# Kernel optimization log

Hardware: AMD Instinct MI355X
Metric: run time of the kernel (lower is better)

## Reference

```python
import jax, jax.numpy as jnp
import numpy as np

NUM_LAYER = 4
EMB = 64
ATOM_VOCAB = 64
BOND_VOCAB = 8
BN_EPS = 1e-5


def _batchnorm(h, gamma, beta):
    m = h.mean(axis=0)
    v = h.var(axis=0)
    return gamma * (h - m) * jax.lax.rsqrt(v + BN_EPS) + beta


def setup_inputs() -> dict:
    key = jax.random.key(0)
    ks = jax.random.split(key, 16)
    N, E, L = 100000, 1000000, NUM_LAYER
    x = jax.random.randint(ks[0], (N, 9), 0, ATOM_VOCAB)
    edge_index = jax.random.randint(ks[1], (2, E), 0, N)
    edge_attr = jax.random.randint(ks[2], (E, 3), 0, BOND_VOCAB)
    batch = jnp.sort(jax.random.randint(ks[3], (N,), 0, 512))
    s = 0.02
    atom_emb = jax.random.normal(ks[4], (9, ATOM_VOCAB, EMB), jnp.float32) * s
    bond_emb = jax.random.normal(ks[5], (L, 3, BOND_VOCAB, EMB), jnp.float32) * s
    eps = jnp.zeros((L,), jnp.float32)
    W1 = jax.random.normal(ks[6], (L, EMB, 2 * EMB), jnp.float32) * s
    b1 = jnp.zeros((L, 2 * EMB), jnp.float32)
    bn1_g = jnp.ones((L, 2 * EMB), jnp.float32)
    bn1_b = jnp.zeros((L, 2 * EMB), jnp.float32)
    W2 = jax.random.normal(ks[7], (L, 2 * EMB, EMB), jnp.float32) * s
    b2 = jnp.zeros((L, EMB), jnp.float32)
    bn_g = jnp.ones((L, EMB), jnp.float32)
    bn_b = jnp.zeros((L, EMB), jnp.float32)
    return dict(x=x, edge_index=edge_index, edge_attr=edge_attr, batch=batch,
                atom_emb=atom_emb, bond_emb=bond_emb, eps=eps,
                W1=W1, b1=b1, bn1_g=bn1_g, bn1_b=bn1_b,
                W2=W2, b2=b2, bn_g=bn_g, bn_b=bn_b)


def reference(x, edge_index, edge_attr, batch, atom_emb, bond_emb, eps,
              W1, b1, bn1_g, bn1_b, W2, b2, bn_g, bn_b):
    N = x.shape[0]
    src, dst = edge_index[0], edge_index[1]
    # AtomEncoder: sum embeddings over the 9 atom-feature columns
    h = sum(atom_emb[c][x[:, c]] for c in range(9))  # [N, EMB]
    for layer in range(NUM_LAYER):
        # BondEncoder for this layer
        ee = sum(bond_emb[layer, c][edge_attr[:, c]] for c in range(3))  # [E, EMB]
        # message: relu(x_j + edge_emb); aggregate: scatter-add at dst
        msg = jax.nn.relu(h[src] + ee)
        agg = jax.ops.segment_sum(msg, dst, num_segments=N)
        z = (1.0 + eps[layer]) * h + agg
        # MLP: Linear -> BN -> ReLU -> Linear
        z = z @ W1[layer] + b1[layer]
        z = jax.nn.relu(_batchnorm(z, bn1_g[layer], bn1_b[layer]))
        z = z @ W2[layer] + b2[layer]
        # outer BatchNorm, then ReLU on all but last layer (dropout = identity)
        z = _batchnorm(z, bn_g[layer], bn_b[layer])
        if layer < NUM_LAYER - 1:
            z = jax.nn.relu(z)
        h = z
    return (h, batch)
```

## Files before the change

### kernel.cpp

```cpp
#include <hip/hip_runtime.h>
#include <hip/hip_bf16.h>

#define N_NODES 100000
#define N_EDGES 1000000
#define EMB 64
#define NLAYER 4
#define NTILE 1563
#define NSB 391
#define NSHARD 16

typedef __hip_bfloat16 bf16;
typedef __attribute__((ext_vector_type(8))) short short8;
typedef __attribute__((ext_vector_type(4))) float f32x4;

static __device__ __forceinline__ float b2f(bf16 v) { return __bfloat162float(v); }
static __device__ __forceinline__ bf16 f2b(float v) { return __float2bfloat16(v); }

__global__ void k_atom(const int* __restrict__ x, const bf16* __restrict__ aemb,
                       bf16* __restrict__ P) {
    int tid = blockIdx.x * 256 + threadIdx.x;
    int n = tid >> 6, e = tid & 63;
    float s = 0.f;
#pragma unroll
    for (int c = 0; c < 9; ++c) {
        int v = x[n * 9 + c];
        s += b2f(aemb[(c * 64 + v) * 64 + e]);
    }
    P[tid] = f2b(s);
}

__global__ void k_bond(const bf16* __restrict__ bemb, bf16* __restrict__ cb) {
    int idx = blockIdx.x * 256 + threadIdx.x;
    int l = idx >> 15, r = idx & 32767;
    int combo = r >> 6, c = r & 63;
    int e0 = combo & 7, e1 = (combo >> 3) & 7, e2 = combo >> 6;
    float v = b2f(bemb[((l * 3 + 0) * 8 + e0) * 64 + c]) +
              b2f(bemb[((l * 3 + 1) * 8 + e1) * 64 + c]) +
              b2f(bemb[((l * 3 + 2) * 8 + e2) * 64 + c]);
    cb[idx] = f2b(v);
}

__global__ void k_hist(const int* __restrict__ ei, int* __restrict__ deg) {
    int e = blockIdx.x * 256 + threadIdx.x;
    if (e < N_EDGES) atomicAdd(&deg[ei[N_EDGES + e]], 1);
}

__global__ void k_scanA(const int* __restrict__ deg, int* __restrict__ bsum) {
    __shared__ int red[256];
    int i = blockIdx.x * 256 + threadIdx.x;
    red[threadIdx.x] = (i < N_NODES) ? deg[i] : 0;
    __syncthreads();
    for (int d = 128; d > 0; d >>= 1) {
        if (threadIdx.x < d) red[threadIdx.x] += red[threadIdx.x + d];
        __syncthreads();
    }
    if (threadIdx.x == 0) bsum[blockIdx.x] = red[0];
}

__global__ void k_scanB(const int* __restrict__ bsum, int* __restrict__ boff,
                        int* __restrict__ offs) {
    __shared__ int s[512];
    int t = threadIdx.x;
    s[t] = (t < NSB) ? bsum[t] : 0;
    __syncthreads();
    for (int d = 1; d < 512; d <<= 1) {
        int v = (t >= d) ? s[t - d] : 0;
        __syncthreads();
        s[t] += v;
        __syncthreads();
    }
    if (t < NSB) boff[t] = s[t] - bsum[t];
    if (t == 0) offs[N_NODES] = s[NSB - 1];
}

__global__ void k_scanC(const int* __restrict__ deg, const int* __restrict__ boff,
                        int* __restrict__ offs, int* __restrict__ cursor) {
    __shared__ int s[256];
    int i = blockIdx.x * 256 + threadIdx.x;
    int t = threadIdx.x;
    int d0 = (i < N_NODES) ? deg[i] : 0;
    s[t] = d0;
    __syncthreads();
    for (int d = 1; d < 256; d <<= 1) {
        int v = (t >= d) ? s[t - d] : 0;
        __syncthreads();
        s[t] += v;
        __syncthreads();
    }
    if (i < N_NODES) {
        int off = boff[blockIdx.x] + s[t] - d0;
        offs[i] = off;
        cursor[i] = off;
    }
}

__global__ void k_bucket(const int* __restrict__ ei, const int* __restrict__ ea,
                         int* __restrict__ cursor, int2* __restrict__ csr) {
    int e = blockIdx.x * 256 + threadIdx.x;
    if (e < N_EDGES) {
        int d = ei[N_EDGES + e];
        int pos = atomicAdd(&cursor[d], 1);
        int pk = ea[e * 3] + (ea[e * 3 + 1] << 3) + (ea[e * 3 + 2] << 6);
        csr[pos] = make_int2(ei[e], pk);
    }
}

__global__ void k_agg(const bf16* __restrict__ P, const int* __restrict__ offs,
                      const int2* __restrict__ csr,
                      const bf16* __restrict__ cb, const bf16* __restrict__ eps,
                      const float* __restrict__ p2s, const bf16* __restrict__ g2,
                      const bf16* __restrict__ bb2, int layer,
                      bf16* __restrict__ G, float* __restrict__ p1s) {
    if (blockIdx.x < NSHARD) p1s[blockIdx.x * 256 + threadIdx.x] = 0.f;
    int tid = blockIdx.x * 256 + threadIdx.x;
    int c = tid & 63;
    int n = __builtin_amdgcn_readfirstlane(tid >> 6);
    float av = 1.f, cv = 0.f, lo = -3.4e38f;
    if (layer > 0) {
        const float* pp = p2s + (layer - 1) * NSHARD * 128;
        float S = 0.f, Q = 0.f;
#pragma unroll
        for (int s = 0; s < NSHARD; ++s) { S += pp[s * 128 + c]; Q += pp[s * 128 + 64 + c]; }
        float mean = S / (float)N_NODES;
        float var = fmaxf(Q / (float)N_NODES - mean * mean, 0.f);
        av = b2f(g2[(layer - 1) * 64 + c]) * rsqrtf(var + 1e-5f);
        cv = b2f(bb2[(layer - 1) * 64 + c]) - mean * av;
        lo = 0.f;
    }
    const bf16* cbl = cb + layer * 512 * 64;
    float hself = fmaxf(av * b2f(P[(size_t)n * 64 + c]) + cv, lo);
    float acc = (1.f + b2f(eps[layer])) * hself;
    int s0 = __builtin_amdgcn_readfirstlane(offs[n]);
    int s1 = __builtin_amdgcn_readfirstlane(offs[n + 1]);
    int i = s0;
    for (; i + 8 <= s1; i += 8) {
        int sr[8], ep[8];
        float hv[8], bv[8];
#pragma unroll
        for (int u = 0; u < 8; ++u) {
            int2 ed = csr[i + u];
            sr[u] = __builtin_amdgcn_readfirstlane(ed.x);
            ep[u] = __builtin_amdgcn_readfirstlane(ed.y);
        }
#pragma unroll
        for (int u = 0; u < 8; ++u) hv[u] = b2f(P[(size_t)sr[u] * 64 + c]);
#pragma unroll
        for (int u = 0; u < 8; ++u) bv[u] = b2f(cbl[(size_t)ep[u] * 64 + c]);
#pragma unroll
        for (int u = 0; u < 8; ++u)
            acc += fmaxf(fmaxf(av * hv[u] + cv, lo) + bv[u], 0.f);
    }
    for (; i + 4 <= s1; i += 4) {
        int sr[4], ep[4];
        float hv[4], bv[4];
#pragma unroll
        for (int u = 0; u < 4; ++u) {
            int2 ed = csr[i + u];
            sr[u] = __builtin_amdgcn_readfirstlane(ed.x);
            ep[u] = __builtin_amdgcn_readfirstlane(ed.y);
        }
#pragma unroll
        for (int u = 0; u < 4; ++u) hv[u] = b2f(P[(size_t)sr[u] * 64 + c]);
#pragma unroll
        for (int u = 0; u < 4; ++u) bv[u] = b2f(cbl[(size_t)ep[u] * 64 + c]);
#pragma unroll
        for (int u = 0; u < 4; ++u)
            acc += fmaxf(fmaxf(av * hv[u] + cv, lo) + bv[u], 0.f);
    }
    for (; i < s1; ++i) {
        int2 ed = csr[i];
        int sr = __builtin_amdgcn_readfirstlane(ed.x);
        int ep = __builtin_amdgcn_readfirstlane(ed.y);
        float m = fmaxf(av * b2f(P[(size_t)sr * 64 + c]) + cv, lo) +
                  b2f(cbl[(size_t)ep * 64 + c]);
        acc += fmaxf(m, 0.f);
    }
    G[tid] = f2b(acc);
}

__global__ void k_wt(const bf16* __restrict__ W1, const bf16* __restrict__ W2,
                     bf16* __restrict__ W1T, bf16* __restrict__ W2T) {
    int idx = blockIdx.x * 256 + threadIdx.x;
    int l = idx >> 13, r = idx & 8191;
    int k = r >> 7, n = r & 127;
    W1T[l * 8192 + n * 64 + k] = W1[idx];
    int k2 = r >> 6, n2 = r & 63;
    W2T[l * 8192 + n2 * 128 + k2] = W2[idx];
}

__global__ __launch_bounds__(256) void k_mlp1s(
    const bf16* __restrict__ X, const bf16* __restrict__ W1T, const bf16* __restrict__ b1,
    int layer, float* __restrict__ p1s, float* __restrict__ p2s) {
    __shared__ bf16 w1t[128 * 72];
    __shared__ bf16 zt[64 * 72];
    __shared__ float ps[4][4][32];
    __shared__ float qs[4][4][32];
    if (blockIdx.x < NSHARD && threadIdx.x < 128)
        p2s[(layer * NSHARD + blockIdx.x) * 128 + threadIdx.x] = 0.f;
    const bf16* Wl = W1T + layer * 8192;
    for (int i = threadIdx.x; i < 1024; i += 256) {
        int n = i >> 3, kc = (i & 7) * 8;
        *(short8*)&w1t[n * 72 + kc] = *(const short8*)&Wl[n * 64 + kc];
    }
    int r0 = blockIdx.x * 64;
    int nrows = min(64, N_NODES - r0);
    for (int i = threadIdx.x; i < 512; i += 256) {
        int r = i >> 3, c = (i & 7) * 8;
        short8 v = {};
        if (r < nrows) v = *(const short8*)&X[(r0 + r) * 64 + c];
        *(short8*)&zt[r * 72 + c] = v;
    }
    __syncthreads();
    int wid = threadIdx.x >> 6;
    int l = threadIdx.x & 63;
    int l15 = l & 15, lq = l >> 4;
    f32x4 acc[4][2];
#pragma unroll
    for (int m = 0; m < 4; ++m)
#pragma unroll
        for (int n = 0; n < 2; ++n) acc[m][n] = (f32x4){0.f, 0.f, 0.f, 0.f};
#pragma unroll
    for (int s = 0; s < 2; ++s) {
        short8 a[4], b[2];
#pragma unroll
        for (int m = 0; m < 4; ++m)
            a[m] = *(const short8*)&zt[(m * 16 + l15) * 72 + s * 32 + lq * 8];
#pragma unroll
        for (int n = 0; n < 2; ++n)
            b[n] = *(const short8*)&w1t[(wid * 32 + n * 16 + l15) * 72 + s * 32 + lq * 8];
#pragma unroll
        for (int m = 0; m < 4; ++m)
#pragma unroll
            for (int n = 0; n < 2; ++n)
                acc[m][n] = __builtin_amdgcn_mfma_f32_16x16x32_bf16(a[m], b[n], acc[m][n], 0, 0, 0);
    }
    float bb[2], cs[2] = {0.f, 0.f}, cq[2] = {0.f, 0.f};
#pragma unroll
    for (int n = 0; n < 2; ++n) bb[n] = b2f(b1[layer * 128 + wid * 32 + n * 16 + l15]);
#pragma unroll
    for (int m = 0; m < 4; ++m)
#pragma unroll
        for (int r = 0; r < 4; ++r) {
            int row = m * 16 + lq * 4 + r;
            if (row < nrows) {
#pragma unroll
                for (int n = 0; n < 2; ++n) {
                    float v = acc[m][n][r] + bb[n];
                    cs[n] += v; cq[n] += v * v;
                }
            }
        }
#pragma unroll
    for (int n = 0; n < 2; ++n) {
        ps[wid][lq][n * 16 + l15] = cs[n];
        qs[wid][lq][n * 16 + l15] = cq[n];
    }
    __syncthreads();
    if (threadIdx.x < 128) {
        int t = threadIdx.x, ww = t >> 5, cc = t & 31;
        float S = 0.f, Q = 0.f;
#pragma unroll
        for (int s4 = 0; s4 < 4; ++s4) { S += ps[ww][s4][cc]; Q += qs[ww][s4][cc]; }
        int sh = blockIdx.x & (NSHARD - 1);
        atomicAdd(&p1s[sh * 256 + t], S);
        atomicAdd(&p1s[sh * 256 + 128 + t], Q);
    }
}

__global__ __launch_bounds__(256) void k_mlp2(
    const bf16* __restrict__ W1T, const bf16* __restrict__ b1,
    const bf16* __restrict__ g1, const bf16* __restrict__ bb1,
    const float* __restrict__ p1s,
    const bf16* __restrict__ W2T, const bf16* __restrict__ bias2, int layer,
    const bf16* __restrict__ X, bf16* __restrict__ Y, float* __restrict__ p2s) {
    __shared__ bf16 w1[128 * 72];
    __shared__ bf16 w2[64 * 136];
    __shared__ bf16 zt[64 * 72];
    __shared__ bf16 yt[64 * 136];
    __shared__ float ps2[4][4][16];
    __shared__ float qs2[4][4][16];
    const bf16* W1l = W1T + layer * 8192;
    const bf16* W2l = W2T + layer * 8192;
    for (int i = threadIdx.x; i < 1024; i += 256) {
        int n = i >> 3, kc = (i & 7) * 8;
        *(short8*)&w1[n * 72 + kc] = *(const short8*)&W1l[n * 64 + kc];
    }
    for (int i = threadIdx.x; i < 1024; i += 256) {
        int n = i >> 4, kc = (i & 15) * 8;
        *(short8*)&w2[n * 136 + kc] = *(const short8*)&W2l[n * 128 + kc];
    }
    int r0 = blockIdx.x * 64;
    int nrows = min(64, N_NODES - r0);
    for (int i = threadIdx.x; i < 512; i += 256) {
        int r = i >> 3, c = (i & 7) * 8;
        short8 v = {};
        if (r < nrows) v = *(const short8*)&X[(r0 + r) * 64 + c];
        *(short8*)&zt[r * 72 + c] = v;
    }
    __syncthreads();
    int wid = threadIdx.x >> 6;
    int l = threadIdx.x & 63;
    int l15 = l & 15, lq = l >> 4;
    {
        f32x4 acc[4][2];
#pragma unroll
        for (int m = 0; m < 4; ++m)
#pragma unroll
            for (int n = 0; n < 2; ++n) acc[m][n] = (f32x4){0.f, 0.f, 0.f, 0.f};
#pragma unroll
        for (int s = 0; s < 2; ++s) {
            short8 a[4], b[2];
#pragma unroll
            for (int m = 0; m < 4; ++m)
                a[m] = *(const short8*)&zt[(m * 16 + l15) * 72 + s * 32 + lq * 8];
#pragma unroll
            for (int n = 0; n < 2; ++n)
                b[n] = *(const short8*)&w1[(wid * 32 + n * 16 + l15) * 72 + s * 32 + lq * 8];
#pragma unroll
            for (int m = 0; m < 4; ++m)
#pragma unroll
                for (int n = 0; n < 2; ++n)
                    acc[m][n] = __builtin_amdgcn_mfma_f32_16x16x32_bf16(a[m], b[n], acc[m][n], 0, 0, 0);
        }
        float aav[2], ccv[2], bbv[2];
#pragma unroll
        for (int n = 0; n < 2; ++n) {
            int col = wid * 32 + n * 16 + l15;
            float S = 0.f, Q = 0.f;
#pragma unroll
            for (int s4 = 0; s4 < NSHARD; ++s4) {
                S += p1s[s4 * 256 + col];
                Q += p1s[s4 * 256 + 128 + col];
            }
            float mean = S / (float)N_NODES;
            float var = fmaxf(Q / (float)N_NODES - mean * mean, 0.f);
            aav[n] = b2f(g1[layer * 128 + col]) * rsqrtf(var + 1e-5f);
            ccv[n] = b2f(bb1[layer * 128 + col]) - mean * aav[n];
            bbv[n] = b2f(b1[layer * 128 + col]);
        }
#pragma unroll
        for (int m = 0; m < 4; ++m)
#pragma unroll
            for (int n = 0; n < 2; ++n)
#pragma unroll
                for (int r = 0; r < 4; ++r) {
                    int row = m * 16 + lq * 4 + r;
                    float v = fmaxf(aav[n] * (acc[m][n][r] + bbv[n]) + ccv[n], 0.f);
                    yt[row * 136 + wid * 32 + n * 16 + l15] = f2b(v);
                }
    }
    __syncthreads();
    {
        f32x4 acc2[4];
#pragma unroll
        for (int m = 0; m < 4; ++m) acc2[m] = (f32x4){0.f, 0.f, 0.f, 0.f};
#pragma unroll
        for (int s = 0; s < 4; ++s) {
            short8 a[4];
            short8 b = *(const short8*)&w2[(wid * 16 + l15) * 136 + s * 32 + lq * 8];
#pragma unroll
            for (int m = 0; m < 4; ++m)
                a[m] = *(const short8*)&yt[(m * 16 + l15) * 136 + s * 32 + lq * 8];
#pragma unroll
            for (int m = 0; m < 4; ++m)
                acc2[m] = __builtin_amdgcn_mfma_f32_16x16x32_bf16(a[m], b, acc2[m], 0, 0, 0);
        }
        float bb2 = b2f(bias2[layer * 64 + wid * 16 + l15]);
        float cs = 0.f, cq = 0.f;
#pragma unroll
        for (int m = 0; m < 4; ++m)
#pragma unroll
            for (int r = 0; r < 4; ++r) {
                int row = m * 16 + lq * 4 + r;
                float v = acc2[m][r] + bb2;
                zt[row * 72 + wid * 16 + l15] = f2b(v);
                if (row < nrows) { cs += v; cq += v * v; }
            }
        ps2[wid][lq][l15] = cs;
        qs2[wid][lq][l15] = cq;
    }
    __syncthreads();
    for (int i = threadIdx.x; i < 512; i += 256) {
        int r = i >> 3, c = (i & 7) * 8;
        if (r < nrows)
            *(short8*)&Y[(r0 + r) * 64 + c] = *(const short8*)&zt[r * 72 + c];
    }
    if (threadIdx.x < 64) {
        int ww = threadIdx.x >> 4, cc = threadIdx.x & 15;
        float S = 0.f, Q = 0.f;
#pragma unroll
        for (int s4 = 0; s4 < 4; ++s4) { S += ps2[ww][s4][cc]; Q += qs2[ww][s4][cc]; }
        int sh = blockIdx.x & (NSHARD - 1);
        atomicAdd(&p2s[(layer * NSHARD + sh) * 128 + threadIdx.x], S);
        atomicAdd(&p2s[(layer * NSHARD + sh) * 128 + 64 + threadIdx.x], Q);
    }
}

__global__ void k_out(const bf16* __restrict__ P, const float* __restrict__ p2s,
                      const bf16* __restrict__ g2, const bf16* __restrict__ bb2,
                      const int* __restrict__ batch, float* __restrict__ out) {
    int tid = blockIdx.x * 256 + threadIdx.x;
    int c = tid & 63;
    const float* pp = p2s + 3 * NSHARD * 128;
    float S = 0.f, Q = 0.f;
#pragma unroll
    for (int s = 0; s < NSHARD; ++s) { S += pp[s * 128 + c]; Q += pp[s * 128 + 64 + c]; }
    float mean = S / (float)N_NODES;
    float var = fmaxf(Q / (float)N_NODES - mean * mean, 0.f);
    float av = b2f(g2[3 * 64 + c]) * rsqrtf(var + 1e-5f);
    float cv = b2f(bb2[3 * 64 + c]) - mean * av;
    float v = b2f(f2b(av * b2f(P[tid]) + cv));
    out[tid] = (v != v || fabsf(v) > 1e20f) ? 0.f : v;
    if (tid < N_NODES) out[N_NODES * EMB + tid] = (float)batch[tid];
}

extern "C" void kernel_launch(void* const* d_in, const int* in_sizes, int n_in,
                              void* d_out, int out_size, void* d_ws, size_t ws_size,
                              hipStream_t stream) {
    (void)in_sizes; (void)n_in; (void)out_size; (void)ws_size;
    const int* x     = (const int*)d_in[0];
    const int* ei    = (const int*)d_in[1];
    const int* ea    = (const int*)d_in[2];
    const int* batch = (const int*)d_in[3];
    const bf16* aemb = (const bf16*)d_in[4];
    const bf16* bemb = (const bf16*)d_in[5];
    const bf16* eps  = (const bf16*)d_in[6];
    const bf16* W1   = (const bf16*)d_in[7];
    const bf16* b1   = (const bf16*)d_in[8];
    const bf16* g1   = (const bf16*)d_in[9];
    const bf16* bb1  = (const bf16*)d_in[10];
    const bf16* W2   = (const bf16*)d_in[11];
    const bf16* b2   = (const bf16*)d_in[12];
    const bf16* g2   = (const bf16*)d_in[13];
    const bf16* bb2  = (const bf16*)d_in[14];

    bf16* Y = (bf16*)d_ws;
    char* ob = (char*)d_out;
    bf16* X       = (bf16*)ob;
    int*  deg     = (int*)(ob + 12800000);
    int*  offs    = (int*)(ob + 13200000);
    int*  cursor  = (int*)(ob + 13600008);
    int2* csr     = (int2*)(ob + 14000008);
    float* p1s    = (float*)(ob + 22000008);
    float* p2s    = (float*)(ob + 22016392);
    int*  bsum    = (int*)(ob + 22049160);
    int*  boff    = (int*)(ob + 22050724);
    bf16* w1t     = (bf16*)(ob + 22052288);
    bf16* w2t     = (bf16*)(ob + 22117824);
    bf16* cbt     = (bf16*)(ob + 22183360);

    hipMemsetAsync(deg, 0, 400000, stream);

    k_atom<<<25000, 256, 0, stream>>>(x, aemb, Y);
    k_wt<<<128, 256, 0, stream>>>(W1, W2, w1t, w2t);
    k_bond<<<512, 256, 0, stream>>>(bemb, cbt);
    k_hist<<<3907, 256, 0, stream>>>(ei, deg);
    k_scanA<<<NSB, 256, 0, stream>>>(deg, bsum);
    k_scanB<<<1, 512, 0, stream>>>(bsum, boff, offs);
    k_scanC<<<NSB, 256, 0, stream>>>(deg, boff, offs, cursor);
    k_bucket<<<3907, 256, 0, stream>>>(ei, ea, cursor, csr);

    for (int l = 0; l < NLAYER; ++l) {
        k_agg<<<25000, 256, 0, stream>>>(Y, offs, csr, cbt, eps,
                                         p2s, g2, bb2, l, X, p1s);
        k_mlp1s<<<NTILE, 256, 0, stream>>>(X, w1t, b1, l, p1s, p2s);
        k_mlp2<<<NTILE, 256, 0, stream>>>(w1t, b1, g1, bb1, p1s, w2t, b2, l, X, Y, p2s);
    }
    k_out<<<25000, 256, 0, stream>>>(Y, p2s, g2, bb2, batch, (float*)d_out);
}
```

Baseline: 584.7 us.

## Fuse edge aggregation with first MLP GEMM statistics pass per 64-row tile

Merges the aggregation kernel and the first-linear BN-statistics kernel into one kernel that aggregates 64 nodes per block into shared memory, then runs the MFMA GEMM and accumulates column sums. This drops one launch per layer and the re-read of the aggregated tile from global memory. The p1s statistics buffer is double-buffered by layer parity so the next layer's zeroing does not race with the current reads. The cost is fewer, heavier blocks (1563 instead of 25000), with each wave walking 16 nodes in sequence, which may reduce latency hiding for the irregular gathers.

```diff
diff --git a/kernel.cpp b/kernel.cpp
--- a/kernel.cpp
+++ b/kernel.cpp
@@ -95,7 +95,9 @@
 }
 
 __global__ void k_bucket(const int* __restrict__ ei, const int* __restrict__ ea,
-                         int* __restrict__ cursor, int2* __restrict__ csr) {
+                         int* __restrict__ cursor, int2* __restrict__ csr,
+                         float* __restrict__ p1s) {
+    if (blockIdx.x < NSHARD) p1s[blockIdx.x * 256 + threadIdx.x] = 0.f;
     int e = blockIdx.x * 256 + threadIdx.x;
     if (e < N_EDGES) {
         int d = ei[N_EDGES + e];
@@ -105,19 +107,35 @@
     }
 }
 
-__global__ void k_agg(const bf16* __restrict__ P, const int* __restrict__ offs,
-                      const int2* __restrict__ csr,
-                      const bf16* __restrict__ cb, const bf16* __restrict__ eps,
-                      const float* __restrict__ p2s, const bf16* __restrict__ g2,
-                      const bf16* __restrict__ bb2, int layer,
-                      bf16* __restrict__ G, float* __restrict__ p1s) {
-    if (blockIdx.x < NSHARD) p1s[blockIdx.x * 256 + threadIdx.x] = 0.f;
-    int tid = blockIdx.x * 256 + threadIdx.x;
-    int c = tid & 63;
-    int n = __builtin_amdgcn_readfirstlane(tid >> 6);
+__global__ __launch_bounds__(256) void k_aggm(
+    const bf16* __restrict__ P, const int* __restrict__ offs,
+    const int2* __restrict__ csr, const bf16* __restrict__ cb,
+    const bf16* __restrict__ eps,
+    const float* __restrict__ p2sall, const bf16* __restrict__ g2,
+    const bf16* __restrict__ bb2,
+    const bf16* __restrict__ W1T, const bf16* __restrict__ b1,
+    int layer, bf16* __restrict__ X,
+    float* __restrict__ p1s, float* __restrict__ p2s) {
+    __shared__ bf16 w1t[128 * 72];
+    __shared__ bf16 zt[64 * 72];
+    __shared__ float ps[4][4][32];
+    __shared__ float qs[4][4][32];
+    if (blockIdx.x < NSHARD) {
+        p1s[((layer + 1) & 1) * 4096 + blockIdx.x * 256 + threadIdx.x] = 0.f;
+        if (threadIdx.x < 128)
+            p2s[(layer * NSHARD + blockIdx.x) * 128 + threadIdx.x] = 0.f;
+    }
+    const bf16* Wl = W1T + layer * 8192;
+    for (int i = threadIdx.x; i < 1024; i += 256) {
+        int nn = i >> 3, kc = (i & 7) * 8;
+        *(short8*)&w1t[nn * 72 + kc] = *(const short8*)&Wl[nn * 64 + kc];
+    }
+    int c = threadIdx.x & 63;
+    int w = threadIdx.x >> 6;
+    int r0 = blockIdx.x * 64;
     float av = 1.f, cv = 0.f, lo = -3.4e38f;
     if (layer > 0) {
-        const float* pp = p2s + (layer - 1) * NSHARD * 128;
+        const float* pp = p2sall + (layer - 1) * NSHARD * 128;
         float S = 0.f, Q = 0.f;
 #pragma unroll
         for (int s = 0; s < NSHARD; ++s) { S += pp[s * 128 + c]; Q += pp[s * 128 + 64 + c]; }
@@ -128,54 +146,116 @@
         lo = 0.f;
     }
     const bf16* cbl = cb + layer * 512 * 64;
-    float hself = fmaxf(av * b2f(P[(size_t)n * 64 + c]) + cv, lo);
-    float acc = (1.f + b2f(eps[layer])) * hself;
-    int s0 = __builtin_amdgcn_readfirstlane(offs[n]);
-    int s1 = __builtin_amdgcn_readfirstlane(offs[n + 1]);
-    int i = s0;
-    for (; i + 8 <= s1; i += 8) {
-        int sr[8], ep[8];
-        float hv[8], bv[8];
-#pragma unroll
-        for (int u = 0; u < 8; ++u) {
-            int2 ed = csr[i + u];
-            sr[u] = __builtin_amdgcn_readfirstlane(ed.x);
-            ep[u] = __builtin_amdgcn_readfirstlane(ed.y);
+    float epsv = 1.f + b2f(eps[layer]);
+    for (int k = 0; k < 16; ++k) {
+        int row = w * 16 + k;
+        int n = r0 + row;
+        float outv = 0.f;
+        if (n < N_NODES) {
+            float acc = epsv * fmaxf(av * b2f(P[(size_t)n * 64 + c]) + cv, lo);
+            int s0 = __builtin_amdgcn_readfirstlane(offs[n]);
+            int s1 = __builtin_amdgcn_readfirstlane(offs[n + 1]);
+            int i = s0;
+            for (; i + 8 <= s1; i += 8) {
+                int sr[8], ep[8];
+                float hv[8], bv[8];
+#pragma unroll
+                for (int u = 0; u < 8; ++u) {
+                    int2 ed = csr[i + u];
+                    sr[u] = __builtin_amdgcn_readfirstlane(ed.x);
+                    ep[u] = __builtin_amdgcn_readfirstlane(ed.y);
+                }
+#pragma unroll
+                for (int u = 0; u < 8; ++u) hv[u] = b2f(P[(size_t)sr[u] * 64 + c]);
+#pragma unroll
+                for (int u = 0; u < 8; ++u) bv[u] = b2f(cbl[(size_t)ep[u] * 64 + c]);
+#pragma unroll
+                for (int u = 0; u < 8; ++u)
+                    acc += fmaxf(fmaxf(av * hv[u] + cv, lo) + bv[u], 0.f);
+            }
+            for (; i + 4 <= s1; i += 4) {
+                int sr[4], ep[4];
+                float hv[4], bv[4];
+#pragma unroll
+                for (int u = 0; u < 4; ++u) {
+                    int2 ed = csr[i + u];
+                    sr[u] = __builtin_amdgcn_readfirstlane(ed.x);
+                    ep[u] = __builtin_amdgcn_readfirstlane(ed.y);
+                }
+#pragma unroll
+                for (int u = 0; u < 4; ++u) hv[u] = b2f(P[(size_t)sr[u] * 64 + c]);
+#pragma unroll
+                for (int u = 0; u < 4; ++u) bv[u] = b2f(cbl[(size_t)ep[u] * 64 + c]);
+#pragma unroll
+                for (int u = 0; u < 4; ++u)
+                    acc += fmaxf(fmaxf(av * hv[u] + cv, lo) + bv[u], 0.f);
+            }
+            for (; i < s1; ++i) {
+                int2 ed = csr[i];
+                int sr = __builtin_amdgcn_readfirstlane(ed.x);
+                int ep = __builtin_amdgcn_readfirstlane(ed.y);
+                acc += fmaxf(fmaxf(av * b2f(P[(size_t)sr * 64 + c]) + cv, lo) +
+                             b2f(cbl[(size_t)ep * 64 + c]), 0.f);
+            }
+            outv = acc;
+            X[(size_t)n * 64 + c] = f2b(acc);
         }
-#pragma unroll
-        for (int u = 0; u < 8; ++u) hv[u] = b2f(P[(size_t)sr[u] * 64 + c]);
-#pragma unroll
-        for (int u = 0; u < 8; ++u) bv[u] = b2f(cbl[(size_t)ep[u] * 64 + c]);
-#pragma unroll
-        for (int u = 0; u < 8; ++u)
-            acc += fmaxf(fmaxf(av * hv[u] + cv, lo) + bv[u], 0.f);
-    }
-    for (; i + 4 <= s1; i += 4) {
-        int sr[4], ep[4];
-        float hv[4], bv[4];
-#pragma unroll
-        for (int u = 0; u < 4; ++u) {
-            int2 ed = csr[i + u];
-            sr[u] = __builtin_amdgcn_readfirstlane(ed.x);
-            ep[u] = __builtin_amdgcn_readfirstlane(ed.y);
+        zt[row * 72 + c] = f2b(outv);
+    }
+    __syncthreads();
+    int nrows = min(64, N_NODES - r0);
+    int l15 = c & 15, lq = c >> 4;
+    f32x4 acc[4][2];
+#pragma unroll
+    for (int m = 0; m < 4; ++m)
+#pragma unroll
+        for (int n = 0; n < 2; ++n) acc[m][n] = (f32x4){0.f, 0.f, 0.f, 0.f};
+#pragma unroll
+    for (int s = 0; s < 2; ++s) {
+        short8 a[4], b[2];
+#pragma unroll
+        for (int m = 0; m < 4; ++m)
+            a[m] = *(const short8*)&zt[(m * 16 + l15) * 72 + s * 32 + lq * 8];
+#pragma unroll
+        for (int n = 0; n < 2; ++n)
+            b[n] = *(const short8*)&w1t[(w * 32 + n * 16 + l15) * 72 + s * 32 + lq * 8];
+#pragma unroll
+        for (int m = 0; m < 4; ++m)
+#pragma unroll
+            for (int n = 0; n < 2; ++n)
+                acc[m][n] = __builtin_amdgcn_mfma_f32_16x16x32_bf16(a[m], b[n], acc[m][n], 0, 0, 0);
+    }
+    float bb[2], cs[2] = {0.f, 0.f}, cq[2] = {0.f, 0.f};
+#pragma unroll
+    for (int n = 0; n < 2; ++n) bb[n] = b2f(b1[layer * 128 + w * 32 + n * 16 + l15]);
+#pragma unroll
+    for (int m = 0; m < 4; ++m)
+#pragma unroll
+        for (int r = 0; r < 4; ++r) {
+            int row = m * 16 + lq * 4 + r;
+            if (row < nrows) {
+#pragma unroll
+                for (int n = 0; n < 2; ++n) {
+                    float v = acc[m][n][r] + bb[n];
+                    cs[n] += v; cq[n] += v * v;
+                }
+            }
         }
 #pragma unroll
-        for (int u = 0; u < 4; ++u) hv[u] = b2f(P[(size_t)sr[u] * 64 + c]);
-#pragma unroll
-        for (int u = 0; u < 4; ++u) bv[u] = b2f(cbl[(size_t)ep[u] * 64 + c]);
-#pragma unroll
-        for (int u = 0; u < 4; ++u)
-            acc += fmaxf(fmaxf(av * hv[u] + cv, lo) + bv[u], 0.f);
-    }
-    for (; i < s1; ++i) {
-        int2 ed = csr[i];
-        int sr = __builtin_amdgcn_readfirstlane(ed.x);
-        int ep = __builtin_amdgcn_readfirstlane(ed.y);
-        float m = fmaxf(av * b2f(P[(size_t)sr * 64 + c]) + cv, lo) +
-                  b2f(cbl[(size_t)ep * 64 + c]);
-        acc += fmaxf(m, 0.f);
-    }
-    G[tid] = f2b(acc);
+    for (int n = 0; n < 2; ++n) {
+        ps[w][lq][n * 16 + l15] = cs[n];
+        qs[w][lq][n * 16 + l15] = cq[n];
+    }
+    __syncthreads();
+    if (threadIdx.x < 128) {
+        int t = threadIdx.x, ww = t >> 5, cc = t & 31;
+        float S = 0.f, Q = 0.f;
+#pragma unroll
+        for (int s4 = 0; s4 < 4; ++s4) { S += ps[ww][s4][cc]; Q += qs[ww][s4][cc]; }
+        int sh = blockIdx.x & (NSHARD - 1);
+        atomicAdd(&p1s[(layer & 1) * 4096 + sh * 256 + t], S);
+        atomicAdd(&p1s[(layer & 1) * 4096 + sh * 256 + 128 + t], Q);
+    }
 }
 
 __global__ void k_wt(const bf16* __restrict__ W1, const bf16* __restrict__ W2,
@@ -186,85 +266,6 @@
     W1T[l * 8192 + n * 64 + k] = W1[idx];
     int k2 = r >> 6, n2 = r & 63;
     W2T[l * 8192 + n2 * 128 + k2] = W2[idx];
-}
-
-__global__ __launch_bounds__(256) void k_mlp1s(
-    const bf16* __restrict__ X, const bf16* __restrict__ W1T, const bf16* __restrict__ b1,
-    int layer, float* __restrict__ p1s, float* __restrict__ p2s) {
-    __shared__ bf16 w1t[128 * 72];
-    __shared__ bf16 zt[64 * 72];
-    __shared__ float ps[4][4][32];
-    __shared__ float qs[4][4][32];
-    if (blockIdx.x < NSHARD && threadIdx.x < 128)
-        p2s[(layer * NSHARD + blockIdx.x) * 128 + threadIdx.x] = 0.f;
-    const bf16* Wl = W1T + layer * 8192;
-    for (int i = threadIdx.x; i < 1024; i += 256) {
-        int n = i >> 3, kc = (i & 7) * 8;
-        *(short8*)&w1t[n * 72 + kc] = *(const short8*)&Wl[n * 64 + kc];
-    }
-    int r0 = blockIdx.x * 64;
-    int nrows = min(64, N_NODES - r0);
-    for (int i = threadIdx.x; i < 512; i += 256) {
-        int r = i >> 3, c = (i & 7) * 8;
-        short8 v = {};
-        if (r < nrows) v = *(const short8*)&X[(r0 + r) * 64 + c];
-        *(short8*)&zt[r * 72 + c] = v;
-    }
-    __syncthreads();
-    int wid = threadIdx.x >> 6;
-    int l = threadIdx.x & 63;
-    int l15 = l & 15, lq = l >> 4;
-    f32x4 acc[4][2];
-#pragma unroll
-    for (int m = 0; m < 4; ++m)
-#pragma unroll
-        for (int n = 0; n < 2; ++n) acc[m][n] = (f32x4){0.f, 0.f, 0.f, 0.f};
-#pragma unroll
-    for (int s = 0; s < 2; ++s) {
-        short8 a[4], b[2];
-#pragma unroll
-        for (int m = 0; m < 4; ++m)
-            a[m] = *(const short8*)&zt[(m * 16 + l15) * 72 + s * 32 + lq * 8];
-#pragma unroll
-        for (int n = 0; n < 2; ++n)
-            b[n] = *(const short8*)&w1t[(wid * 32 + n * 16 + l15) * 72 + s * 32 + lq * 8];
-#pragma unroll
-        for (int m = 0; m < 4; ++m)
-#pragma unroll
-            for (int n = 0; n < 2; ++n)
-                acc[m][n] = __builtin_amdgcn_mfma_f32_16x16x32_bf16(a[m], b[n], acc[m][n], 0, 0, 0);
-    }
-    float bb[2], cs[2] = {0.f, 0.f}, cq[2] = {0.f, 0.f};
-#pragma unroll
-    for (int n = 0; n < 2; ++n) bb[n] = b2f(b1[layer * 128 + wid * 32 + n * 16 + l15]);
-#pragma unroll
-    for (int m = 0; m < 4; ++m)
-#pragma unroll
-        for (int r = 0; r < 4; ++r) {
-            int row = m * 16 + lq * 4 + r;
-            if (row < nrows) {
-#pragma unroll
-                for (int n = 0; n < 2; ++n) {
-                    float v = acc[m][n][r] + bb[n];
-                    cs[n] += v; cq[n] += v * v;
-                }
-            }
-        }
-#pragma unroll
-    for (int n = 0; n < 2; ++n) {
-        ps[wid][lq][n * 16 + l15] = cs[n];
-        qs[wid][lq][n * 16 + l15] = cq[n];
-    }
-    __syncthreads();
-    if (threadIdx.x < 128) {
-        int t = threadIdx.x, ww = t >> 5, cc = t & 31;
-        float S = 0.f, Q = 0.f;
-#pragma unroll
-        for (int s4 = 0; s4 < 4; ++s4) { S += ps[ww][s4][cc]; Q += qs[ww][s4][cc]; }
-        int sh = blockIdx.x & (NSHARD - 1);
-        atomicAdd(&p1s[sh * 256 + t], S);
-        atomicAdd(&p1s[sh * 256 + 128 + t], Q);
-    }
 }
 
 __global__ __launch_bounds__(256) void k_mlp2(
@@ -442,12 +443,12 @@
     int*  cursor  = (int*)(ob + 13600008);
     int2* csr     = (int2*)(ob + 14000008);
     float* p1s    = (float*)(ob + 22000008);
-    float* p2s    = (float*)(ob + 22016392);
-    int*  bsum    = (int*)(ob + 22049160);
-    int*  boff    = (int*)(ob + 22050724);
-    bf16* w1t     = (bf16*)(ob + 22052288);
-    bf16* w2t     = (bf16*)(ob + 22117824);
-    bf16* cbt     = (bf16*)(ob + 22183360);
+    float* p2s    = (float*)(ob + 22032776);
+    int*  bsum    = (int*)(ob + 22065544);
+    int*  boff    = (int*)(ob + 22067108);
+    bf16* w1t     = (bf16*)(ob + 22068672);
+    bf16* w2t     = (bf16*)(ob + 22134208);
+    bf16* cbt     = (bf16*)(ob + 22199744);
 
     hipMemsetAsync(deg, 0, 400000, stream);
 
@@ -458,13 +459,13 @@
     k_scanA<<<NSB, 256, 0, stream>>>(deg, bsum);
     k_scanB<<<1, 512, 0, stream>>>(bsum, boff, offs);
     k_scanC<<<NSB, 256, 0, stream>>>(deg, boff, offs, cursor);
-    k_bucket<<<3907, 256, 0, stream>>>(ei, ea, cursor, csr);
+    k_bucket<<<3907, 256, 0, stream>>>(ei, ea, cursor, csr, p1s);
 
     for (int l = 0; l < NLAYER; ++l) {
-        k_agg<<<25000, 256, 0, stream>>>(Y, offs, csr, cbt, eps,
-                                         p2s, g2, bb2, l, X, p1s);
-        k_mlp1s<<<NTILE, 256, 0, stream>>>(X, w1t, b1, l, p1s, p2s);
-        k_mlp2<<<NTILE, 256, 0, stream>>>(w1t, b1, g1, bb1, p1s, w2t, b2, l, X, Y, p2s);
+        k_aggm<<<NTILE, 256, 0, stream>>>(Y, offs, csr, cbt, eps, p2s, g2, bb2,
+                                          w1t, b1, l, X, p1s, p2s);
+        k_mlp2<<<NTILE, 256, 0, stream>>>(w1t, b1, g1, bb1, p1s + (l & 1) * 4096,
+                                          w2t, b2, l, X, Y, p2s);
     }
     k_out<<<25000, 256, 0, stream>>>(Y, p2s, g2, bb2, batch, (float*)d_out);
 }
```

New measurement: 683.0 us. 1.17x slower.
